# Performance work log

Hardware: AMD Instinct MI355X
Metric: run time of the kernel (lower is better)

The kernel has to match this reference:

```python
import math
import jax, jax.numpy as jnp
import numpy as np

D_MODEL = 1024
N_HEADS = 16
HEAD_DIM = D_MODEL // N_HEADS
WINDOW = 1024
BATCH = 2
SEQ = 2048


def _alibi_slopes(n_heads):
    # power-of-2 branch of ALiBiPositionalEmbedding._get_slopes
    start = 2 ** (-2 ** (-(math.log2(n_heads) - 3)))
    return jnp.asarray([start * start ** i for i in range(n_heads)], dtype=jnp.float32)


def setup_inputs() -> dict:
    key = jax.random.key(0)
    ks = jax.random.split(key, 5)
    scale = 0.02
    return {
        "x": jax.random.normal(ks[0], (BATCH, SEQ, D_MODEL), dtype=jnp.float32),
        "wq": jax.random.normal(ks[1], (D_MODEL, D_MODEL), dtype=jnp.float32) * scale,
        "bq": jnp.zeros((D_MODEL,), dtype=jnp.float32),
        "wk": jax.random.normal(ks[2], (D_MODEL, D_MODEL), dtype=jnp.float32) * scale,
        "bk": jnp.zeros((D_MODEL,), dtype=jnp.float32),
        "wv": jax.random.normal(ks[3], (D_MODEL, D_MODEL), dtype=jnp.float32) * scale,
        "bv": jnp.zeros((D_MODEL,), dtype=jnp.float32),
        "wo": jax.random.normal(ks[4], (D_MODEL, D_MODEL), dtype=jnp.float32) * scale,
        "bo": jnp.zeros((D_MODEL,), dtype=jnp.float32),
    }


def reference(x, wq, bq, wk, bk, wv, bv, wo, bo):
    B, S, _ = x.shape
    # projections (torch Linear: y = x @ W.T + b)
    q = (x @ wq.T + bq).reshape(B, S, N_HEADS, HEAD_DIM).transpose(0, 2, 1, 3)
    k = (x @ wk.T + bk).reshape(B, S, N_HEADS, HEAD_DIM).transpose(0, 2, 1, 3)
    v = (x @ wv.T + bv).reshape(B, S, N_HEADS, HEAD_DIM).transpose(0, 2, 1, 3)

    scores = jnp.einsum("bhqd,bhkd->bhqk", q, k) / math.sqrt(HEAD_DIM)

    # ALiBi bias: -|i-j| * slope_h, shape [H, S, S]
    pos = jnp.arange(S)
    slopes = _alibi_slopes(N_HEADS)  # [H]
    pos_diff = -jnp.abs(pos[None, :] - pos[:, None]).astype(scores.dtype)  # [S,S]
    scores = scores + pos_diff[None, None, :, :] * slopes[None, :, None, None]

    # causal + sliding-window mask: allow row-WINDOW < col <= row
    row = pos[:, None]
    col = pos[None, :]
    mask = (col > row) | (col <= row - WINDOW)  # [S,S] True = masked out
    neg = jnp.finfo(scores.dtype).min
    scores = jnp.where(mask[None, None, :, :], neg, scores)

    probs = jax.nn.softmax(scores, axis=-1)
    out = jnp.einsum("bhqk,bhkd->bhqd", probs, v)  # [B,H,S,D]
    out = out.transpose(0, 2, 1, 3).reshape(B, S, D_MODEL)
    return out @ wo.T + bo
```

## Files before the change

kernel.cpp:

```cpp
#include <hip/hip_runtime.h>
#include <cstdint>
#include <cstddef>

#define S_LEN 2048
#define NH 16
#define HD 64
#define DM 1024
#define WIN 1024

typedef unsigned short u16;
typedef __attribute__((ext_vector_type(8))) short bf16x8;
typedef __attribute__((ext_vector_type(4))) short bf16x4;
typedef __attribute__((ext_vector_type(4))) float f32x4;
typedef __attribute__((ext_vector_type(4))) u16 u16x4;
typedef __attribute__((ext_vector_type(2))) uint32_t u32x2;
typedef __attribute__((ext_vector_type(4))) uint32_t u32x4;

__device__ inline u16 f2b(float f) {
  union { float f; uint32_t u; } x; x.f = f;
  uint32_t r = x.u + 0x7FFFu + ((x.u >> 16) & 1u);
  return (u16)(r >> 16);
}

__device__ inline uint32_t cvt_pk_bf16(float a, float b) {
  uint32_t r;
  asm("v_cvt_pk_bf16_f32 %0, %1, %2" : "=v"(r) : "v"(a), "v"(b));
  return r;
}

__device__ inline void gload16(const void* g, void* l) {
  __builtin_amdgcn_global_load_lds((const __attribute__((address_space(1))) void*)g,
                                   (__attribute__((address_space(3))) void*)l, 16, 0, 0);
}

__global__ __launch_bounds__(256)
void cvt_all(const float* __restrict__ x,
             const float* __restrict__ wq, const float* __restrict__ wk,
             const float* __restrict__ wv, const float* __restrict__ wo,
             u16* __restrict__ xb, u16* __restrict__ wqkvb, u16* __restrict__ wob) {
  size_t i = ((size_t)blockIdx.x * 256 + threadIdx.x) * 4;
  const float* src; u16* dst;
  if (i < 4194304) {
    src = x + i; dst = xb + i;
  } else {
    size_t j = i - 4194304;
    int w = (int)(j >> 20);
    size_t off = j & 1048575;
    switch (w) {
      case 0:  src = wq + off; dst = wqkvb + off; break;
      case 1:  src = wk + off; dst = wqkvb + 1048576 + off; break;
      case 2:  src = wv + off; dst = wqkvb + 2097152 + off; break;
      default: src = wo + off; dst = wob + off; break;
    }
  }
  f32x4 v = *(const f32x4*)src;
  u16x4 o;
  o[0] = f2b(v[0]); o[1] = f2b(v[1]); o[2] = f2b(v[2]); o[3] = f2b(v[3]);
  *(u16x4*)dst = o;
}

template<int EPI>
__global__ __launch_bounds__(256, 4)
void gemm_nt(const u16* __restrict__ A, const u16* __restrict__ B,
             const float* __restrict__ b0, const float* __restrict__ b1,
             const float* __restrict__ b2,
             float* __restrict__ outF, u16* __restrict__ outQ,
             int M, int N, int K) {
  __shared__ u16 As[128 * 64];
  __shared__ u16 Bs[128 * 64];
  const int t = threadIdx.x;
  const int lane = t & 63, wid = t >> 6;
  const int l15 = lane & 15, l4 = lane >> 4;
  const int x = l15 & 7;
  const int wr = wid >> 1, wc = wid & 1;
  const int bmB = M >> 7, bnB = N >> 7;
  const int stripe = bmB >> 3;
  const int per = stripe * bnB;
  const int job = (blockIdx.x & 7) * per + (blockIdx.x >> 3);
  const int r_ = job % per;
  const int bm = ((job / per) * stripe + r_ / bnB) << 7;
  const int bn = (r_ % bnB) << 7;
  const int srow0 = t >> 3;
  const int colx = ((t * 16) & 127) ^ (((t >> 3) & 7) << 4);
  const char* Ap = (const char*)A + ((size_t)(bm + srow0) * K) * 2 + colx;
  const char* Bp = (const char*)B + ((size_t)(bn + srow0) * K) * 2 + colx;
  const size_t sstr = (size_t)32 * K * 2;
  char* Asd = (char*)As + t * 16;
  char* Bsd = (char*)Bs + t * 16;
  f32x4 acc[4][4];
#pragma unroll
  for (int i = 0; i < 4; i++)
#pragma unroll
    for (int j = 0; j < 4; j++) acc[i][j] = (f32x4){0.f, 0.f, 0.f, 0.f};

  for (int kb = 0; kb < K; kb += 64) {
    __syncthreads();
#pragma unroll
    for (int shot = 0; shot < 4; shot++) {
      gload16(Ap + (size_t)kb * 2 + shot * sstr, Asd + shot * 4096);
      gload16(Bp + (size_t)kb * 2 + shot * sstr, Bsd + shot * 4096);
    }
    __syncthreads();
#pragma unroll
    for (int ks2 = 0; ks2 < 2; ks2++) {
      bf16x8 af[4], bq[4];
#pragma unroll
      for (int mi = 0; mi < 4; mi++)
        af[mi] = *(bf16x8*)&As[(wr * 64 + mi * 16 + l15) * 64 +
                               (((ks2 * 4 + l4) ^ x) << 3)];
#pragma unroll
      for (int ni = 0; ni < 4; ni++)
        bq[ni] = *(bf16x8*)&Bs[(wc * 64 + ni * 16 + l15) * 64 +
                               (((ks2 * 4 + l4) ^ x) << 3)];
#pragma unroll
      for (int mi = 0; mi < 4; mi++)
#pragma unroll
        for (int ni = 0; ni < 4; ni++)
          acc[mi][ni] = __builtin_amdgcn_mfma_f32_16x16x32_bf16(af[mi], bq[ni], acc[mi][ni], 0, 0, 0);
    }
  }

  const int cb = bn >> 10;
  const float* bp = (EPI == 0) ? b0 : (cb == 0 ? b0 : (cb == 1 ? b1 : b2));
#pragma unroll
  for (int mi = 0; mi < 4; mi++) {
#pragma unroll
    for (int ni = 0; ni < 4; ni++) {
#pragma unroll
      for (int r = 0; r < 4; r++) {
        int row = bm + wr * 64 + mi * 16 + l4 * 4 + r;
        int col = bn + wc * 64 + ni * 16 + l15;
        float v = acc[mi][ni][r] + bp[col & (DM - 1)];
        if (EPI == 0) {
          outF[(size_t)row * N + col] = v;
        } else {
          int b = row >> 11, s = row & (S_LEN - 1);
          int which = col >> 10, cw = col & (DM - 1);
          int h = cw >> 6, d = cw & (HD - 1);
          outQ[(size_t)which * 4194304 +
               (((size_t)(b * NH + h)) * S_LEN + s) * HD + d] = f2b(v);
        }
      }
    }
  }
}

__global__ __launch_bounds__(256)
void transpose_v(const u16* __restrict__ V, u16* __restrict__ Vt) {
  const int bh = blockIdx.y;
  const int s0 = blockIdx.x * 64;
  __shared__ u16 tile[64][72];
  const int t = threadIdx.x;
  const u16* src = V + ((size_t)bh * S_LEN + s0) * HD;
#pragma unroll
  for (int i = 0; i < 2; i++) {
    int e = t * 8 + i * 2048;
    int r = e >> 6, c = e & 63;
    *(bf16x8*)&tile[r][c] = *(const bf16x8*)(src + e);
  }
  __syncthreads();
  u16* dst = Vt + (size_t)bh * HD * S_LEN + s0;
#pragma unroll
  for (int i = 0; i < 2; i++) {
    int e = t * 8 + i * 2048;
    int d = e >> 6, s = e & 63;
    bf16x8 tmp;
#pragma unroll
    for (int j = 0; j < 8; j++) tmp[j] = (short)tile[s + j][d];
    *(bf16x8*)&dst[(size_t)d * S_LEN + s] = tmp;
  }
}

__device__ __forceinline__ void stage_tiles(const char* __restrict__ Kg,
                                            const char* __restrict__ Vg,
                                            u16* __restrict__ Kl, u16* __restrict__ Vl,
                                            int t) {
#pragma unroll
  for (int shot = 0; shot < 2; shot++) {
    int o = shot * 4096 + t * 16;
    int sw = ((o >> 7) & 7) << 4;
    gload16(Kg + (o ^ sw), (char*)Kl + o);
    gload16(Vg + (size_t)(o >> 7) * 4096 + ((o & 127) ^ sw), (char*)Vl + o);
  }
}

__device__ __forceinline__ void process_tile16(
    int kb, const u16* __restrict__ Kl, const u16* __restrict__ Vl,
    const bf16x8 qf[2], const float c16[16],
    int qw, int l15, int hi, float slope2, float qks,
    float& lsum, f32x4 O[4]) {
  const int x = l15 & 7;
  f32x4 st[4];
#pragma unroll
  for (int f = 0; f < 4; f++) st[f] = (f32x4){0.f, 0.f, 0.f, 0.f};
#pragma unroll
  for (int ks = 0; ks < 2; ks++)
#pragma unroll
    for (int f = 0; f < 4; f++) {
      bf16x8 kf = *(const bf16x8*)&Kl[(16 * f + l15) * 64 + (((4 * ks + hi) ^ x) << 3)];
      st[f] = __builtin_amdgcn_mfma_f32_16x16x32_bf16(kf, qf[ks], st[f], 0, 0, 0);
    }

  const int dkb = kb + 4 * hi - (qw + l15);
  const float base = slope2 * (float)dkb - 8.f;
  const bool interior = (kb + 63 <= qw) && (kb - (qw + 15) > -WIN);
  float p[16];
  if (interior) {
#pragma unroll
    for (int f = 0; f < 4; f++)
#pragma unroll
      for (int r = 0; r < 4; r++)
        p[4 * f + r] = fmaf(st[f][r], qks, base + c16[4 * f + r]);
  } else {
#pragma unroll
    for (int f = 0; f < 4; f++)
#pragma unroll
      for (int r = 0; r < 4; r++) {
        int dk = dkb + 16 * f + r;
        float s = fmaf(st[f][r], qks, base + c16[4 * f + r]);
        p[4 * f + r] = (dk > 0 || dk <= -WIN) ? -3e38f : s;
      }
  }

#pragma unroll
  for (int r = 0; r < 16; r++) p[r] = exp2f(p[r]);
  float a8[8];
#pragma unroll
  for (int r = 0; r < 8; r++) a8[r] = p[r] + p[r + 8];
#pragma unroll
  for (int r = 0; r < 4; r++) a8[r] += a8[r + 4];
  lsum += (a8[0] + a8[1]) + (a8[2] + a8[3]);

  bf16x8 pb[2];
#pragma unroll
  for (int kc = 0; kc < 2; kc++) {
    u32x4 w4;
    w4[0] = cvt_pk_bf16(p[8 * kc + 0], p[8 * kc + 1]);
    w4[1] = cvt_pk_bf16(p[8 * kc + 2], p[8 * kc + 3]);
    w4[2] = cvt_pk_bf16(p[8 * kc + 4], p[8 * kc + 5]);
    w4[3] = cvt_pk_bf16(p[8 * kc + 6], p[8 * kc + 7]);
    pb[kc] = __builtin_bit_cast(bf16x8, w4);
  }

#pragma unroll
  for (int d = 0; d < 4; d++) {
#pragma unroll
    for (int kc = 0; kc < 2; kc++) {
      const int row = (16 * d + l15) * 64;
      bf16x4 a = *(const bf16x4*)&Vl[row + (((4 * kc + (hi >> 1)) ^ x) << 3) + 4 * (hi & 1)];
      bf16x4 bql = *(const bf16x4*)&Vl[row + (((4 * kc + 2 + (hi >> 1)) ^ x) << 3) + 4 * (hi & 1)];
      bf16x8 vf;
      vf[0] = a[0]; vf[1] = a[1]; vf[2] = a[2]; vf[3] = a[3];
      vf[4] = bql[0]; vf[5] = bql[1]; vf[6] = bql[2]; vf[7] = bql[3];
      O[d] = __builtin_amdgcn_mfma_f32_16x16x32_bf16(vf, pb[kc], O[d], 0, 0, 0);
    }
  }
}

__global__ __launch_bounds__(256, 4)
void attn_kernel(const u16* __restrict__ Q, const u16* __restrict__ Kg,
                 const u16* __restrict__ Vt, u16* __restrict__ attn) {
  __shared__ __align__(16) u16 Klds[2][4096];
  __shared__ __align__(16) u16 Vlds[2][4096];
  const int bid = blockIdx.x;
  const int job = (bid & 7) * 128 + (bid >> 3);
  const int bh = job >> 5;
  const int qb = ((31 - (job & 31)) + (bh << 3)) & 31;
  const int b = bh >> 4, h = bh & 15;
  const int tid = threadIdx.x;
  const int wid = tid >> 6, lane = tid & 63;
  const int l15 = lane & 15, hi = lane >> 4;
  const int q0 = qb << 6;
  const int qw = q0 + 16 * wid;
  const u16* Qp = Q + (size_t)bh * (S_LEN * HD);
  const char* Kbase = (const char*)(Kg + (size_t)bh * (S_LEN * HD));
  const char* Vbase = (const char*)(Vt + (size_t)bh * (HD * S_LEN));

  bf16x8 qf[2];
#pragma unroll
  for (int ks = 0; ks < 2; ks++)
    qf[ks] = *(const bf16x8*)(Qp + (size_t)(qw + l15) * HD + 32 * ks + 8 * hi);

  const float slope2 = exp2f(-0.5f * (float)(h + 1)) * 1.44269504f;
  const float qks = 0.125f * 1.44269504f;
  float c16[16];
#pragma unroll
  for (int f = 0; f < 4; f++)
#pragma unroll
    for (int r = 0; r < 4; r++) c16[4 * f + r] = slope2 * (float)(16 * f + r);

  float lsum = 0.f;
  f32x4 O[4];
#pragma unroll
  for (int d = 0; d < 4; d++) O[d] = (f32x4){0.f, 0.f, 0.f, 0.f};

  int lo_u = q0 - (WIN - 1); if (lo_u < 0) lo_u = 0; lo_u &= ~63;
  const int hi_u = q0;
  int lo_w = qw - (WIN - 1); if (lo_w < 0) lo_w = 0; lo_w &= ~63;
  const int last_w = (qw + 15) & ~63;

  stage_tiles(Kbase + (size_t)lo_u * 128, Vbase + (size_t)lo_u * 2,
              Klds[0], Vlds[0], tid);
  int cur = 0;
  for (int kb = lo_u; kb <= hi_u; kb += 64) {
    __syncthreads();
    if (kb + 64 <= hi_u)
      stage_tiles(Kbase + (size_t)(kb + 64) * 128, Vbase + (size_t)(kb + 64) * 2,
                  Klds[cur ^ 1], Vlds[cur ^ 1], tid);
    if (kb >= lo_w && kb <= last_w)
      process_tile16(kb, Klds[cur], Vlds[cur], qf, c16,
                     qw, l15, hi, slope2, qks, lsum, O);
    cur ^= 1;
  }

  lsum += __shfl_xor(lsum, 16, 64);
  lsum += __shfl_xor(lsum, 32, 64);

  const float invl = 1.f / lsum;
  u16* op = attn + ((size_t)(b * S_LEN) + qw + l15) * DM + h * HD + 4 * hi;
#pragma unroll
  for (int d = 0; d < 4; d++) {
    u32x2 w;
    w[0] = cvt_pk_bf16(O[d][0] * invl, O[d][1] * invl);
    w[1] = cvt_pk_bf16(O[d][2] * invl, O[d][3] * invl);
    *(u32x2*)(op + d * 16) = w;
  }
}

extern "C" void kernel_launch(void* const* d_in, const int* in_sizes, int n_in,
                              void* d_out, int out_size, void* d_ws, size_t ws_size,
                              hipStream_t stream) {
  const float* x  = (const float*)d_in[0];
  const float* wq = (const float*)d_in[1];
  const float* bq = (const float*)d_in[2];
  const float* wk = (const float*)d_in[3];
  const float* bk = (const float*)d_in[4];
  const float* wv = (const float*)d_in[5];
  const float* bv = (const float*)d_in[6];
  const float* wo = (const float*)d_in[7];
  const float* bo = (const float*)d_in[8];

  char* ws = (char*)d_ws;
  u16* xb    = (u16*)(ws);
  u16* wqkvb = (u16*)(ws + 8388608);
  u16* wob   = (u16*)(ws + 14680064);
  u16* QKVb  = (u16*)(ws + 16777216);
  u16* Vtb   = (u16*)(ws + 41943040);
  u16* Ab    = (u16*)(ws + 50331648);
  u16* Vb    = QKVb + 2 * 4194304;

  const int M = 4096;

  cvt_all<<<dim3(8192), dim3(256), 0, stream>>>(x, wq, wk, wv, wo,
                                                xb, wqkvb, wob);

  gemm_nt<1><<<dim3(768), dim3(256), 0, stream>>>(xb, wqkvb, bq, bk, bv,
                                                  nullptr, QKVb, M, 3072, DM);

  transpose_v<<<dim3(32, 32), dim3(256), 0, stream>>>(Vb, Vtb);

  attn_kernel<<<dim3(1024), dim3(256), 0, stream>>>(QKVb, QKVb + 4194304, Vtb, Ab);

  gemm_nt<0><<<dim3(256), dim3(256), 0, stream>>>(Ab, wob, bo, nullptr, nullptr,
                                                  (float*)d_out, nullptr, M, DM, DM);
}
```

Baseline: 107.5 us.

## Compute V transposed directly via swapped-operand GEMM, drop transpose kernel

```diff
diff --git a/kernel.cpp b/kernel.cpp
--- a/kernel.cpp
+++ b/kernel.cpp
@@ -121,7 +121,7 @@
   }
 
   const int cb = bn >> 10;
-  const float* bp = (EPI == 0) ? b0 : (cb == 0 ? b0 : (cb == 1 ? b1 : b2));
+  const float* bp = (EPI == 1) ? (cb == 0 ? b0 : b1) : b0;
 #pragma unroll
   for (int mi = 0; mi < 4; mi++) {
 #pragma unroll
@@ -130,44 +130,24 @@
       for (int r = 0; r < 4; r++) {
         int row = bm + wr * 64 + mi * 16 + l4 * 4 + r;
         int col = bn + wc * 64 + ni * 16 + l15;
-        float v = acc[mi][ni][r] + bp[col & (DM - 1)];
         if (EPI == 0) {
+          float v = acc[mi][ni][r] + bp[col];
           outF[(size_t)row * N + col] = v;
-        } else {
+        } else if (EPI == 1) {
+          float v = acc[mi][ni][r] + bp[col & (DM - 1)];
           int b = row >> 11, s = row & (S_LEN - 1);
           int which = col >> 10, cw = col & (DM - 1);
           int h = cw >> 6, d = cw & (HD - 1);
           outQ[(size_t)which * 4194304 +
                (((size_t)(b * NH + h)) * S_LEN + s) * HD + d] = f2b(v);
+        } else {
+          float v = acc[mi][ni][r] + bp[row];
+          int b = col >> 11, s = col & (S_LEN - 1);
+          int h = row >> 6, d = row & (HD - 1);
+          outQ[(((size_t)(b * NH + h)) * HD + d) * S_LEN + s] = f2b(v);
         }
       }
     }
-  }
-}
-
-__global__ __launch_bounds__(256)
-void transpose_v(const u16* __restrict__ V, u16* __restrict__ Vt) {
-  const int bh = blockIdx.y;
-  const int s0 = blockIdx.x * 64;
-  __shared__ u16 tile[64][72];
-  const int t = threadIdx.x;
-  const u16* src = V + ((size_t)bh * S_LEN + s0) * HD;
-#pragma unroll
-  for (int i = 0; i < 2; i++) {
-    int e = t * 8 + i * 2048;
-    int r = e >> 6, c = e & 63;
-    *(bf16x8*)&tile[r][c] = *(const bf16x8*)(src + e);
-  }
-  __syncthreads();
-  u16* dst = Vt + (size_t)bh * HD * S_LEN + s0;
-#pragma unroll
-  for (int i = 0; i < 2; i++) {
-    int e = t * 8 + i * 2048;
-    int d = e >> 6, s = e & 63;
-    bf16x8 tmp;
-#pragma unroll
-    for (int j = 0; j < 8; j++) tmp[j] = (short)tile[s + j][d];
-    *(bf16x8*)&dst[(size_t)d * S_LEN + s] = tmp;
   }
 }
 
@@ -347,17 +327,18 @@
   u16* QKVb  = (u16*)(ws + 16777216);
   u16* Vtb   = (u16*)(ws + 41943040);
   u16* Ab    = (u16*)(ws + 50331648);
-  u16* Vb    = QKVb + 2 * 4194304;
+  u16* wvb   = wqkvb + 2097152;
 
   const int M = 4096;
 
   cvt_all<<<dim3(8192), dim3(256), 0, stream>>>(x, wq, wk, wv, wo,
                                                 xb, wqkvb, wob);
 
-  gemm_nt<1><<<dim3(768), dim3(256), 0, stream>>>(xb, wqkvb, bq, bk, bv,
-                                                  nullptr, QKVb, M, 3072, DM);
-
-  transpose_v<<<dim3(32, 32), dim3(256), 0, stream>>>(Vb, Vtb);
+  gemm_nt<1><<<dim3(512), dim3(256), 0, stream>>>(xb, wqkvb, bq, bk, nullptr,
+                                                  nullptr, QKVb, M, 2048, DM);
+
+  gemm_nt<2><<<dim3(256), dim3(256), 0, stream>>>(wvb, xb, bv, nullptr, nullptr,
+                                                  nullptr, Vtb, DM, M, DM);
 
   attn_kernel<<<dim3(1024), dim3(256), 0, stream>>>(QKVb, QKVb + 4194304, Vtb, Ab);
 
```

New measurement: 113.3 us. 1.05x slower.
